# Optimization experiments

Measured on AMD Instinct MI355X. Metric: run time of the kernel, lower is better.

Reference implementation:

```python
import jax, jax.numpy as jnp
import numpy as np

N_HEADS = 4
N_GROUPS = 32
EPS = 1e-5


def setup_inputs() -> dict:
    key = jax.random.key(0)
    ks = jax.random.split(key, 6)
    c = 512
    x = jax.random.normal(ks[0], (4, c, 64, 64), dtype=jnp.float32)
    # conv1x1 weights ~ kaiming-ish scale
    s = 1.0 / np.sqrt(c)
    wq = jax.random.normal(ks[1], (c, c), dtype=jnp.float32) * s
    wk = jax.random.normal(ks[2], (c, c), dtype=jnp.float32) * s
    wv = jax.random.normal(ks[3], (c, c), dtype=jnp.float32) * s
    wp = jax.random.normal(ks[4], (c, c), dtype=jnp.float32) * s
    zeros = jnp.zeros((c,), dtype=jnp.float32)
    return {
        "x": x,
        "gn_w": jnp.ones((c,), dtype=jnp.float32), "gn_b": zeros,
        "wq": wq, "bq": zeros, "wk": wk, "bk": zeros,
        "wv": wv, "bv": zeros, "wp": wp, "bp": zeros,
    }


def _group_norm(x, w, b):
    bsz, c, h, wd = x.shape
    xg = x.reshape(bsz, N_GROUPS, c // N_GROUPS, h, wd)
    mean = xg.mean(axis=(2, 3, 4), keepdims=True)
    var = xg.var(axis=(2, 3, 4), keepdims=True)
    xg = (xg - mean) * jax.lax.rsqrt(var + EPS)
    x = xg.reshape(bsz, c, h, wd)
    return x * w[None, :, None, None] + b[None, :, None, None]


def _conv1x1(x, w, b):
    # x: (b,c,h,w), w: (out,in) -> (b,out,h,w)
    return jnp.einsum('bchw,oc->bohw', x, w) + b[None, :, None, None]


def reference(x, gn_w, gn_b, wq, bq, wk, bk, wv, bv, wp, bp):
    bsz, c, h, wd = x.shape
    hd = c // N_HEADS
    hw = h * wd
    x_n = _group_norm(x, gn_w, gn_b)
    q = _conv1x1(x_n, wq, bq)
    k = _conv1x1(x_n, wk, bk)
    v = _conv1x1(x_n, wv, bv)

    def to_heads(t):
        # (b,c,h,w) -> (b, n_heads, hw, head_dim)
        return t.reshape(bsz, N_HEADS, hd, hw).transpose(0, 1, 3, 2)

    q, k, v = to_heads(q), to_heads(k), to_heads(v)
    scale = hd ** (-0.5)
    attn = jnp.einsum('bhqd,bhkd->bhqk', q, k) * scale  # (b,H,hw,hw)
    attn = jax.nn.softmax(attn, axis=-1)
    out = jnp.einsum('bhqk,bhkd->bhqd', attn, v)
    out = out.transpose(0, 1, 3, 2).reshape(bsz, c, h, wd)
    out = _conv1x1(out, wp, bp)
    return x + out
```

## Files before the change

### kernel.cpp

```cpp
#include <hip/hip_runtime.h>
#include <math.h>

typedef __attribute__((ext_vector_type(8))) short short8;
typedef __attribute__((ext_vector_type(4))) float floatx4;
typedef __attribute__((ext_vector_type(16))) float floatx16;
typedef __attribute__((ext_vector_type(8))) unsigned short ushort8v;
typedef __attribute__((ext_vector_type(4))) unsigned short ushort4v;

#define HW 4096
#define CCH 512
#define NB 4
#define NH 4
#define HD 128

__device__ __forceinline__ unsigned short f2bf(float f) {
    union { float f; unsigned int u; } c; c.f = f;
    unsigned int u = c.u;
    u += 0x7FFFu + ((u >> 16) & 1u);
    return (unsigned short)(u >> 16);
}

__device__ __forceinline__ void gload_lds16(const unsigned short* g, unsigned short* l) {
    __builtin_amdgcn_global_load_lds(
        (const __attribute__((address_space(1))) unsigned int*)g,
        (__attribute__((address_space(3))) unsigned int*)l, 16, 0, 0);
}

__device__ __forceinline__ float sum16(const floatx16& s) {
    return ((((s[0] + s[1]) + (s[2] + s[3])) + ((s[4] + s[5]) + (s[6] + s[7])))
          + (((s[8] + s[9]) + (s[10] + s[11])) + ((s[12] + s[13]) + (s[14] + s[15]))));
}

__global__ void conv_w(const float* __restrict__ w0, const float* __restrict__ w1,
                       const float* __restrict__ w2, const float* __restrict__ w3,
                       unsigned short* __restrict__ dst) {
    const float* src = blockIdx.y == 0 ? w0 : blockIdx.y == 1 ? w1 : blockIdx.y == 2 ? w2 : w3;
    unsigned short* d = dst + (size_t)blockIdx.y * 262144;
    int i = blockIdx.x * 256 + threadIdx.x;
    float4 v = ((const float4*)src)[i];
    ushort4v o;
    o[0] = f2bf(v.x); o[1] = f2bf(v.y); o[2] = f2bf(v.z); o[3] = f2bf(v.w);
    ((ushort4v*)d)[i] = o;
}

__global__ void gn_stats(const float* __restrict__ x, float* __restrict__ stats) {
    int bg = blockIdx.x;
    int b = bg >> 5, g = bg & 31;
    const float4* p = (const float4*)(x + ((size_t)b * CCH + g * 16) * HW);
    float s = 0.f, ss = 0.f;
    for (int i = threadIdx.x; i < 16384; i += 256) {
        float4 v = p[i];
        s  += v.x + v.y + v.z + v.w;
        ss += v.x * v.x + v.y * v.y + v.z * v.z + v.w * v.w;
    }
    #pragma unroll
    for (int off = 32; off > 0; off >>= 1) {
        s  += __shfl_down(s, off, 64);
        ss += __shfl_down(ss, off, 64);
    }
    __shared__ float sm[4], sm2[4];
    int wid = threadIdx.x >> 6;
    if ((threadIdx.x & 63) == 0) { sm[wid] = s; sm2[wid] = ss; }
    __syncthreads();
    if (threadIdx.x == 0) {
        float ts = sm[0] + sm[1] + sm[2] + sm[3];
        float tss = sm2[0] + sm2[1] + sm2[2] + sm2[3];
        float mean = ts * (1.f / 65536.f);
        float var = tss * (1.f / 65536.f) - mean * mean;
        stats[bg * 2] = mean;
        stats[bg * 2 + 1] = rsqrtf(var + 1e-5f);
    }
}

__global__ void gn_apply(const float* __restrict__ x, const float* __restrict__ gnw,
                         const float* __restrict__ gnb, const float* __restrict__ stats,
                         unsigned short* __restrict__ xt) {
    int s = blockIdx.x * 256 + threadIdx.x;
    int g = blockIdx.y, b = blockIdx.z;
    float mean = stats[(b * 32 + g) * 2];
    float rstd = stats[(b * 32 + g) * 2 + 1];
    const float* xb = x + ((size_t)b * CCH + g * 16) * HW + s;
    unsigned short outv[16];
    #pragma unroll
    for (int cl = 0; cl < 16; cl++) {
        int c = g * 16 + cl;
        float v = xb[(size_t)cl * HW];
        v = (v - mean) * rstd * gnw[c] + gnb[c];
        outv[cl] = f2bf(v);
    }
    unsigned short* dst = xt + ((size_t)b * HW + s) * CCH + g * 16;
    *(ushort8v*)dst       = *(ushort8v*)&outv[0];
    *(ushort8v*)(dst + 8) = *(ushort8v*)&outv[8];
}

#define LDP 72
template <int MODE>
__global__ __launch_bounds__(256, 2) void gemm_nt(
    const unsigned short* __restrict__ A, long long aStride,
    const unsigned short* __restrict__ Bm, long long bStride,
    const float* __restrict__ bias, float scale,
    const float* __restrict__ resid, long long rStride,
    void* __restrict__ Cp, long long cStride, int ldc) {
    __shared__ unsigned short lA[2][128 * LDP];
    __shared__ unsigned short lB[2][128 * LDP];
    const int tid = threadIdx.x;
    const int lane = tid & 63;
    const int wid = tid >> 6;
    const int z = blockIdx.z;
    const unsigned short* Ab = A + (size_t)z * aStride + (size_t)blockIdx.x * 128 * 512;
    const unsigned short* Bb = Bm + (size_t)z * bStride + (size_t)blockIdx.y * 128 * 512;

    floatx4 acc[4][4];
    #pragma unroll
    for (int i = 0; i < 4; i++)
        #pragma unroll
        for (int j = 0; j < 4; j++) acc[i][j] = (floatx4)0.f;

    const int wm = (wid >> 1) * 64;
    const int wn = (wid & 1) * 64;
    const int l15 = lane & 15;
    const int l4 = lane >> 4;
    const int srow = tid >> 3;
    const int skc  = (tid & 7) * 8;

    ushort8v ar[4], br[4];
    #pragma unroll
    for (int i = 0; i < 4; i++) {
        int row = srow + i * 32;
        ar[i] = *(const ushort8v*)&Ab[(size_t)row * 512 + skc];
        br[i] = *(const ushort8v*)&Bb[(size_t)row * 512 + skc];
    }
    #pragma unroll
    for (int i = 0; i < 4; i++) {
        int row = srow + i * 32;
        *(ushort8v*)&lA[0][row * LDP + skc] = ar[i];
        *(ushort8v*)&lB[0][row * LDP + skc] = br[i];
    }
    __syncthreads();

    int cur = 0;
    #pragma unroll 1
    for (int t = 0; t < 8; t++) {
        if (t < 7) {
            int k0 = (t + 1) * 64;
            #pragma unroll
            for (int i = 0; i < 4; i++) {
                int row = srow + i * 32;
                ar[i] = *(const ushort8v*)&Ab[(size_t)row * 512 + k0 + skc];
                br[i] = *(const ushort8v*)&Bb[(size_t)row * 512 + k0 + skc];
            }
        }
        #pragma unroll
        for (int kk = 0; kk < 2; kk++) {
            short8 af[4], bf[4];
            #pragma unroll
            for (int i = 0; i < 4; i++)
                af[i] = *(const short8*)&lA[cur][(wm + i * 16 + l15) * LDP + kk * 32 + l4 * 8];
            #pragma unroll
            for (int j = 0; j < 4; j++)
                bf[j] = *(const short8*)&lB[cur][(wn + j * 16 + l15) * LDP + kk * 32 + l4 * 8];
            #pragma unroll
            for (int i = 0; i < 4; i++)
                #pragma unroll
                for (int j = 0; j < 4; j++)
                    acc[i][j] = __builtin_amdgcn_mfma_f32_16x16x32_bf16(af[i], bf[j], acc[i][j], 0, 0, 0);
        }
        if (t < 7) {
            int nxt = cur ^ 1;
            #pragma unroll
            for (int i = 0; i < 4; i++) {
                int row = srow + i * 32;
                *(ushort8v*)&lA[nxt][row * LDP + skc] = ar[i];
                *(ushort8v*)&lB[nxt][row * LDP + skc] = br[i];
            }
            __syncthreads();
            cur = nxt;
        }
    }

    long long m0 = (long long)blockIdx.x * 128 + wm;
    long long n0 = (long long)blockIdx.y * 128 + wn;
    if (MODE == 0 || MODE == 3) {
        unsigned short* C = (unsigned short*)Cp + (size_t)z * cStride;
        const float* bptr = (MODE == 3 && z == 1) ? resid : bias;
        float sc = (MODE == 3 && z == 1) ? 1.f : scale;
        #pragma unroll
        for (int i = 0; i < 4; i++)
            #pragma unroll
            for (int j = 0; j < 4; j++) {
                long long col = n0 + j * 16 + l15;
                float bv = bptr[col];
                #pragma unroll
                for (int r = 0; r < 4; r++) {
                    long long row = m0 + i * 16 + l4 * 4 + r;
                    C[row * ldc + col] = f2bf((acc[i][j][r] + bv) * sc);
                }
            }
    } else if (MODE == 1) {
        float* C = (float*)Cp + (size_t)z * cStride;
        const float* R = resid + (size_t)z * rStride;
        #pragma unroll
        for (int i = 0; i < 4; i++)
            #pragma unroll
            for (int j = 0; j < 4; j++)
                #pragma unroll
                for (int r = 0; r < 4; r++) {
                    long long row = m0 + i * 16 + l4 * 4 + r;
                    long long col = n0 + j * 16 + l15;
                    C[row * ldc + col] = acc[i][j][r] + bias[row] + R[row * ldc + col];
                }
    } else {
        unsigned short* C = (unsigned short*)Cp + (size_t)z * cStride;
        #pragma unroll
        for (int i = 0; i < 4; i++)
            #pragma unroll
            for (int j = 0; j < 4; j++)
                #pragma unroll
                for (int r = 0; r < 4; r++) {
                    long long row = m0 + i * 16 + l4 * 4 + r;
                    long long col = n0 + j * 16 + l15;
                    C[row * ldc + col] = f2bf(acc[i][j][r] + bias[row]);
                }
    }
}

__global__ __launch_bounds__(256, 2) void attn_kern(
    const unsigned short* __restrict__ Qb, const unsigned short* __restrict__ Kb,
    const unsigned short* __restrict__ Vt, unsigned short* __restrict__ Ob) {
    __shared__ __align__(16) unsigned short lk0[8192], lk1[8192];
    __shared__ __align__(16) unsigned short lv0[8192], lv1[8192];
    const int tid = threadIdx.x;
    const int lane = tid & 63;
    const int w = tid >> 6;
    const int l31 = lane & 31;
    const int l1 = lane >> 5;
    const int q0 = blockIdx.x * 128;
    const int h = blockIdx.y, b = blockIdx.z;
    const size_t headOff = (size_t)h * HD;
    const size_t batchRow = (size_t)b * HW;
    const unsigned short* VtB = Vt + ((size_t)b * CCH + headOff) * HW;

    size_t kSrc[4], vSrc[4];
    #pragma unroll
    for (int n = 0; n < 4; n++) {
        int row = w * 16 + n * 4 + (lane >> 4);
        int sk = ((row & 7) << 1) | ((row >> 3) & 1);
        int jk = (lane & 15) ^ sk;
        kSrc[n] = (batchRow + row) * 512 + headOff + jk * 8;
        int d = w * 32 + n * 8 + (lane >> 3);
        int jv = (lane & 7) ^ (d & 7);
        vSrc[n] = (size_t)d * HW + jv * 8;
    }
    const int ldsOff = w * 4 * 512;

    const int sk0 = ((l31 & 7) << 1) | ((l31 >> 3) & 1);
    const int sv0 = l31 & 7;

    short8 qf[8];
    #pragma unroll
    for (int kd = 0; kd < 8; kd++)
        qf[kd] = *(const short8*)&Qb[(batchRow + q0 + w * 32 + l31) * 512
                                     + headOff + kd * 16 + l1 * 8];

    floatx16 acc_o[4];
    #pragma unroll
    for (int dj = 0; dj < 4; dj++) acc_o[dj] = (floatx16)0.f;
    float lsum_part = 0.f;

    #pragma unroll
    for (int n = 0; n < 4; n++) gload_lds16(&Kb[kSrc[n]], lk0 + ldsOff + n * 512);
    #pragma unroll
    for (int n = 0; n < 4; n++) gload_lds16(&Kb[kSrc[n] + (size_t)64 * 512], lk1 + ldsOff + n * 512);
    #pragma unroll
    for (int n = 0; n < 4; n++) gload_lds16(&VtB[vSrc[n]], lv0 + ldsOff + n * 512);
    __syncthreads();

    floatx16 saA0 = (floatx16)0.f, saA1 = (floatx16)0.f;
    floatx16 saB0, saB1;
    #pragma unroll
    for (int kd = 0; kd < 8; kd++) {
        int xk = ((kd * 2 + l1) ^ sk0) * 8;
        short8 kf0 = *(const short8*)&lk0[l31 * 128 + xk];
        short8 kf1 = *(const short8*)&lk0[l31 * 128 + xk + 4096];
        saA0 = __builtin_amdgcn_mfma_f32_32x32x16_bf16(kf0, qf[kd], saA0, 0, 0, 0);
        saA1 = __builtin_amdgcn_mfma_f32_32x32x16_bf16(kf1, qf[kd], saA1, 0, 0, 0);
    }
    __syncthreads();

    unsigned short* lvCur = lv0;  unsigned short* lvNxt = lv1;
    unsigned short* kRead = lk1;  unsigned short* kWrite = lk0;

    auto pack_pv = [&](floatx16& s0, floatx16& s1) {
        #pragma unroll
        for (int r = 0; r < 16; r++) s0[r] = __builtin_amdgcn_exp2f(s0[r]);
        #pragma unroll
        for (int r = 0; r < 16; r++) s1[r] = __builtin_amdgcn_exp2f(s1[r]);
        lsum_part += sum16(s0) + sum16(s1);
        short8 paf[4];
        #pragma unroll
        for (int tb = 0; tb < 2; tb++) {
            const floatx16& sa = tb ? s1 : s0;
            unsigned int wv[4][2];
            #pragma unroll
            for (int g = 0; g < 4; g++) {
                asm("v_cvt_pk_bf16_f32 %0, %1, %2" : "=v"(wv[g][0])
                    : "v"(sa[4 * g + 0]), "v"(sa[4 * g + 1]));
                asm("v_cvt_pk_bf16_f32 %0, %1, %2" : "=v"(wv[g][1])
                    : "v"(sa[4 * g + 2]), "v"(sa[4 * g + 3]));
            }
            #pragma unroll
            for (int hh = 0; hh < 2; hh++) {
                unsigned int a0 = wv[2 * hh][0], b0 = wv[2 * hh + 1][0];
                unsigned int a1 = wv[2 * hh][1], b1 = wv[2 * hh + 1][1];
                asm("v_permlane32_swap_b32 %0, %1" : "+v"(a0), "+v"(b0));
                asm("v_permlane32_swap_b32 %0, %1" : "+v"(a1), "+v"(b1));
                union { unsigned int u[4]; short8 s8; } f;
                f.u[0] = a0; f.u[1] = a1; f.u[2] = b0; f.u[3] = b1;
                paf[2 * tb + hh] = f.s8;
            }
        }
        #pragma unroll
        for (int u = 0; u < 4; u++) {
            int xv = ((u * 2 + l1) ^ sv0) * 8;
            #pragma unroll
            for (int dj = 0; dj < 4; dj++) {
                short8 vv = *(const short8*)&lvCur[dj * 2048 + l31 * 64 + xv];
                acc_o[dj] = __builtin_amdgcn_mfma_f32_32x32x16_bf16(paf[u], vv, acc_o[dj], 0, 0, 0);
            }
        }
    };

    auto step = [&](int kt, floatx16& sO0, floatx16& sO1, floatx16& sN0, floatx16& sN1) {
        size_t tv = (size_t)(kt + 1) * 64;
        size_t tk = (size_t)(kt + 2) * 64 * 512;
        #pragma unroll
        for (int n = 0; n < 4; n++) gload_lds16(&VtB[vSrc[n] + tv], lvNxt + ldsOff + n * 512);
        #pragma unroll
        for (int n = 0; n < 4; n++) gload_lds16(&Kb[kSrc[n] + tk], kWrite + ldsOff + n * 512);

        sN0 = (floatx16)0.f; sN1 = (floatx16)0.f;
        __builtin_amdgcn_s_setprio(1);
        #pragma unroll
        for (int kd = 0; kd < 8; kd++) {
            int xk = ((kd * 2 + l1) ^ sk0) * 8;
            short8 kf0 = *(const short8*)&kRead[l31 * 128 + xk];
            short8 kf1 = *(const short8*)&kRead[l31 * 128 + xk + 4096];
            sN0 = __builtin_amdgcn_mfma_f32_32x32x16_bf16(kf0, qf[kd], sN0, 0, 0, 0);
            sN1 = __builtin_amdgcn_mfma_f32_32x32x16_bf16(kf1, qf[kd], sN1, 0, 0, 0);
        }
        pack_pv(sO0, sO1);
        __builtin_amdgcn_s_setprio(0);

        __syncthreads();
        unsigned short* t_;
        t_ = lvCur; lvCur = lvNxt; lvNxt = t_;
        t_ = kRead; kRead = kWrite; kWrite = t_;
    };

    #pragma unroll 1
    for (int it = 0; it < 31; it++) {
        step(2 * it,     saA0, saA1, saB0, saB1);
        step(2 * it + 1, saB0, saB1, saA0, saA1);
    }
    step(62, saA0, saA1, saB0, saB1);
    pack_pv(saB0, saB1);

    float tot;
    {
        union { float f; unsigned int u; } ua, ub;
        ua.f = lsum_part; ub.f = lsum_part;
        asm("v_permlane32_swap_b32 %0, %1" : "+v"(ua.u), "+v"(ub.u));
        tot = ua.f + ub.f;
    }

    #pragma unroll
    for (int g = 0; g < 4; g++)
        #pragma unroll
        for (int p = 0; p < 4; p++) {
            int reg = 4 * g + p;
            int qr = p + 8 * g + 4 * l1;
            float rl = 1.f / __shfl(tot, qr, 64);
            size_t row = batchRow + q0 + w * 32 + qr;
            #pragma unroll
            for (int dj = 0; dj < 4; dj++)
                Ob[row * 512 + headOff + dj * 32 + l31] = f2bf(acc_o[dj][reg] * rl);
        }
}

extern "C" void kernel_launch(void* const* d_in, const int* in_sizes, int n_in,
                              void* d_out, int out_size, void* d_ws, size_t ws_size,
                              hipStream_t stream) {
    const float* x   = (const float*)d_in[0];
    const float* gnw = (const float*)d_in[1];
    const float* gnb = (const float*)d_in[2];
    const float* wq  = (const float*)d_in[3];
    const float* bq  = (const float*)d_in[4];
    const float* wk  = (const float*)d_in[5];
    const float* bk  = (const float*)d_in[6];
    const float* wv  = (const float*)d_in[7];
    const float* bv  = (const float*)d_in[8];
    const float* wp  = (const float*)d_in[9];
    const float* bp  = (const float*)d_in[10];
    float* out = (float*)d_out;

    const size_t NE = (size_t)NB * HW * CCH;
    unsigned short* ws16 = (unsigned short*)d_ws;
    unsigned short* XT = ws16;
    unsigned short* Qb = ws16 + NE;
    unsigned short* Kb = ws16 + 2 * NE;
    unsigned short* Vt = ws16 + 3 * NE;
    unsigned short* Wb = ws16 + 4 * NE;
    float* stats = (float*)(ws16 + 4 * NE + 4 * 262144);

    const float qscale = 0.08838834764831845f * 1.4426950408889634f;

    conv_w<<<dim3(256, 4), 256, 0, stream>>>(wq, wk, wv, wp, Wb);
    gn_stats<<<128, 256, 0, stream>>>(x, stats);
    gn_apply<<<dim3(16, 32, 4), 256, 0, stream>>>(x, gnw, gnb, stats, XT);

    gemm_nt<3><<<dim3(128, 4, 2), 256, 0, stream>>>(XT, 0, Wb, 262144, bq, qscale, bk, 0,
                                                    Qb, (long long)NE, 512);
    gemm_nt<2><<<dim3(4, 32, 4), 256, 0, stream>>>(Wb + 2 * 262144, 0, XT, (long long)HW * 512, bv, 1.f,
                                                   nullptr, 0, Vt, (long long)CCH * HW, HW);

    unsigned short* Ob = XT;
    attn_kern<<<dim3(32, NH, NB), 256, 0, stream>>>(Qb, Kb, Vt, Ob);

    gemm_nt<1><<<dim3(4, 32, 4), 256, 0, stream>>>(Wb + 3 * 262144, 0, Ob, (long long)HW * 512, bp, 1.f,
                                                   x, (long long)CCH * HW, out, (long long)CCH * HW, HW);
}
```

Measured before the change: 336.9 us.

## Write K in fragment-native layout and load K directly into registers

The QKV projection epilogue now writes K into a per-head, MFMA-fragment-ordered layout, so the attention kernel can load K fragments straight from global memory into registers instead of staging them through LDS. The K LDS buffers and their swizzle are removed, and the two-stage software pipeline (overlapping QK^T of the next tile with softmax/PV of the current) is replaced by a simple loop that prefetches next K into registers during the exp/PV work. This cuts LDS traffic and capacity but raises register pressure, and it loses the explicit QK/PV overlap across tiles. The scattered K epilogue stores may also be less coalesced.

Result: slower. 370.4 us (+10.0%).

```diff
diff --git a/kernel.cpp b/kernel.cpp
--- a/kernel.cpp
+++ b/kernel.cpp
@@ -180,20 +180,38 @@
 
     long long m0 = (long long)blockIdx.x * 128 + wm;
     long long n0 = (long long)blockIdx.y * 128 + wn;
-    if (MODE == 0 || MODE == 3) {
-        unsigned short* C = (unsigned short*)Cp + (size_t)z * cStride;
-        const float* bptr = (MODE == 3 && z == 1) ? resid : bias;
-        float sc = (MODE == 3 && z == 1) ? 1.f : scale;
+    if (MODE == 3 && blockIdx.z == 1) {
+        unsigned short* C = (unsigned short*)Cp + (size_t)cStride;
+        const int hh = blockIdx.y;
         #pragma unroll
         for (int i = 0; i < 4; i++)
             #pragma unroll
             for (int j = 0; j < 4; j++) {
                 long long col = n0 + j * 16 + l15;
-                float bv = bptr[col];
+                float bv = resid[col];
+                int d = (int)(col - (long long)hh * 128);
+                size_t dpart = (size_t)((d >> 4) * 2 + ((d >> 3) & 1)) * 256 + (size_t)(d & 7);
                 #pragma unroll
                 for (int r = 0; r < 4; r++) {
                     long long row = m0 + i * 16 + l4 * 4 + r;
-                    C[row * ldc + col] = f2bf((acc[i][j][r] + bv) * sc);
+                    int bb = (int)(row >> 12), s = (int)(row & 4095);
+                    size_t addr = ((size_t)(bb * NH + hh)) * ((size_t)HW * HD)
+                                + (size_t)(s >> 5) * 4096 + dpart + (size_t)(s & 31) * 8;
+                    C[addr] = f2bf(acc[i][j][r] + bv);
+                }
+            }
+    } else if (MODE == 0 || MODE == 3) {
+        unsigned short* C = (unsigned short*)Cp + (size_t)z * cStride;
+        #pragma unroll
+        for (int i = 0; i < 4; i++)
+            #pragma unroll
+            for (int j = 0; j < 4; j++) {
+                long long col = n0 + j * 16 + l15;
+                float bv = bias[col];
+                #pragma unroll
+                for (int r = 0; r < 4; r++) {
+                    long long row = m0 + i * 16 + l4 * 4 + r;
+                    C[row * ldc + col] = f2bf((acc[i][j][r] + bv) * scale);
                 }
             }
     } else if (MODE == 1) {
@@ -225,9 +243,8 @@
 }
 
 __global__ __launch_bounds__(256, 2) void attn_kern(
-    const unsigned short* __restrict__ Qb, const unsigned short* __restrict__ Kb,
+    const unsigned short* __restrict__ Qb, const unsigned short* __restrict__ Kf,
     const unsigned short* __restrict__ Vt, unsigned short* __restrict__ Ob) {
-    __shared__ __align__(16) unsigned short lk0[8192], lk1[8192];
     __shared__ __align__(16) unsigned short lv0[8192], lv1[8192];
     const int tid = threadIdx.x;
     const int lane = tid & 63;
@@ -239,21 +256,16 @@
     const size_t headOff = (size_t)h * HD;
     const size_t batchRow = (size_t)b * HW;
     const unsigned short* VtB = Vt + ((size_t)b * CCH + headOff) * HW;
-
-    size_t kSrc[4], vSrc[4];
+    const unsigned short* KfB = Kf + (size_t)(b * NH + h) * ((size_t)HW * HD);
+
+    size_t vSrc[4];
     #pragma unroll
     for (int n = 0; n < 4; n++) {
-        int row = w * 16 + n * 4 + (lane >> 4);
-        int sk = ((row & 7) << 1) | ((row >> 3) & 1);
-        int jk = (lane & 15) ^ sk;
-        kSrc[n] = (batchRow + row) * 512 + headOff + jk * 8;
         int d = w * 32 + n * 8 + (lane >> 3);
         int jv = (lane & 7) ^ (d & 7);
         vSrc[n] = (size_t)d * HW + jv * 8;
     }
     const int ldsOff = w * 4 * 512;
-
-    const int sk0 = ((l31 & 7) << 1) | ((l31 >> 3) & 1);
     const int sv0 = l31 & 7;
 
     short8 qf[8];
@@ -268,38 +280,55 @@
     float lsum_part = 0.f;
 
     #pragma unroll
-    for (int n = 0; n < 4; n++) gload_lds16(&Kb[kSrc[n]], lk0 + ldsOff + n * 512);
-    #pragma unroll
-    for (int n = 0; n < 4; n++) gload_lds16(&Kb[kSrc[n] + (size_t)64 * 512], lk1 + ldsOff + n * 512);
-    #pragma unroll
     for (int n = 0; n < 4; n++) gload_lds16(&VtB[vSrc[n]], lv0 + ldsOff + n * 512);
+    short8 kf0[8], kf1[8];
+    {
+        const unsigned short* kb = KfB + lane * 8;
+        #pragma unroll
+        for (int kd = 0; kd < 8; kd++) {
+            kf0[kd] = *(const short8*)(kb + kd * 512);
+            kf1[kd] = *(const short8*)(kb + 4096 + kd * 512);
+        }
+    }
     __syncthreads();
 
-    floatx16 saA0 = (floatx16)0.f, saA1 = (floatx16)0.f;
-    floatx16 saB0, saB1;
-    #pragma unroll
-    for (int kd = 0; kd < 8; kd++) {
-        int xk = ((kd * 2 + l1) ^ sk0) * 8;
-        short8 kf0 = *(const short8*)&lk0[l31 * 128 + xk];
-        short8 kf1 = *(const short8*)&lk0[l31 * 128 + xk + 4096];
-        saA0 = __builtin_amdgcn_mfma_f32_32x32x16_bf16(kf0, qf[kd], saA0, 0, 0, 0);
-        saA1 = __builtin_amdgcn_mfma_f32_32x32x16_bf16(kf1, qf[kd], saA1, 0, 0, 0);
-    }
-    __syncthreads();
-
     unsigned short* lvCur = lv0;  unsigned short* lvNxt = lv1;
-    unsigned short* kRead = lk1;  unsigned short* kWrite = lk0;
-
-    auto pack_pv = [&](floatx16& s0, floatx16& s1) {
-        #pragma unroll
-        for (int r = 0; r < 16; r++) s0[r] = __builtin_amdgcn_exp2f(s0[r]);
-        #pragma unroll
-        for (int r = 0; r < 16; r++) s1[r] = __builtin_amdgcn_exp2f(s1[r]);
-        lsum_part += sum16(s0) + sum16(s1);
+
+    #pragma unroll 1
+    for (int kt = 0; kt < 64; kt++) {
+        if (kt < 63) {
+            size_t tv = (size_t)(kt + 1) * 64;
+            #pragma unroll
+            for (int n = 0; n < 4; n++) gload_lds16(&VtB[vSrc[n] + tv], lvNxt + ldsOff + n * 512);
+        }
+
+        floatx16 sa0 = (floatx16)0.f, sa1 = (floatx16)0.f;
+        __builtin_amdgcn_s_setprio(1);
+        #pragma unroll
+        for (int kd = 0; kd < 8; kd++) {
+            sa0 = __builtin_amdgcn_mfma_f32_32x32x16_bf16(kf0[kd], qf[kd], sa0, 0, 0, 0);
+            sa1 = __builtin_amdgcn_mfma_f32_32x32x16_bf16(kf1[kd], qf[kd], sa1, 0, 0, 0);
+        }
+        __builtin_amdgcn_s_setprio(0);
+
+        if (kt < 63) {
+            const unsigned short* kb = KfB + (size_t)(kt + 1) * 8192 + lane * 8;
+            #pragma unroll
+            for (int kd = 0; kd < 8; kd++) {
+                kf0[kd] = *(const short8*)(kb + kd * 512);
+                kf1[kd] = *(const short8*)(kb + 4096 + kd * 512);
+            }
+        }
+
         short8 paf[4];
         #pragma unroll
+        for (int r = 0; r < 16; r++) sa0[r] = __builtin_amdgcn_exp2f(sa0[r]);
+        #pragma unroll
+        for (int r = 0; r < 16; r++) sa1[r] = __builtin_amdgcn_exp2f(sa1[r]);
+        lsum_part += sum16(sa0) + sum16(sa1);
+        #pragma unroll
         for (int tb = 0; tb < 2; tb++) {
-            const floatx16& sa = tb ? s1 : s0;
+            const floatx16& sa = tb ? sa1 : sa0;
             unsigned int wv[4][2];
             #pragma unroll
             for (int g = 0; g < 4; g++) {
@@ -319,6 +348,8 @@
                 paf[2 * tb + hh] = f.s8;
             }
         }
+
+        __builtin_amdgcn_s_setprio(1);
         #pragma unroll
         for (int u = 0; u < 4; u++) {
             int xv = ((u * 2 + l1) ^ sv0) * 8;
@@ -328,42 +359,13 @@
                 acc_o[dj] = __builtin_amdgcn_mfma_f32_32x32x16_bf16(paf[u], vv, acc_o[dj], 0, 0, 0);
             }
         }
-    };
-
-    auto step = [&](int kt, floatx16& sO0, floatx16& sO1, floatx16& sN0, floatx16& sN1) {
-        size_t tv = (size_t)(kt + 1) * 64;
-        size_t tk = (size_t)(kt + 2) * 64 * 512;
-        #pragma unroll
-        for (int n = 0; n < 4; n++) gload_lds16(&VtB[vSrc[n] + tv], lvNxt + ldsOff + n * 512);
-        #pragma unroll
-        for (int n = 0; n < 4; n++) gload_lds16(&Kb[kSrc[n] + tk], kWrite + ldsOff + n * 512);
-
-        sN0 = (floatx16)0.f; sN1 = (floatx16)0.f;
-        __builtin_amdgcn_s_setprio(1);
-        #pragma unroll
-        for (int kd = 0; kd < 8; kd++) {
-            int xk = ((kd * 2 + l1) ^ sk0) * 8;
-            short8 kf0 = *(const short8*)&kRead[l31 * 128 + xk];
-            short8 kf1 = *(const short8*)&kRead[l31 * 128 + xk + 4096];
-            sN0 = __builtin_amdgcn_mfma_f32_32x32x16_bf16(kf0, qf[kd], sN0, 0, 0, 0);
-            sN1 = __builtin_amdgcn_mfma_f32_32x32x16_bf16(kf1, qf[kd], sN1, 0, 0, 0);
-        }
-        pack_pv(sO0, sO1);
         __builtin_amdgcn_s_setprio(0);
 
-        __syncthreads();
-        unsigned short* t_;
-        t_ = lvCur; lvCur = lvNxt; lvNxt = t_;
-        t_ = kRead; kRead = kWrite; kWrite = t_;
-    };
-
-    #pragma unroll 1
-    for (int it = 0; it < 31; it++) {
-        step(2 * it,     saA0, saA1, saB0, saB1);
-        step(2 * it + 1, saB0, saB1, saA0, saA1);
-    }
-    step(62, saA0, saA1, saB0, saB1);
-    pack_pv(saB0, saB1);
+        if (kt < 63) {
+            __syncthreads();
+            unsigned short* t_ = lvCur; lvCur = lvNxt; lvNxt = t_;
+        }
+    }
 
     float tot;
     {
```
